# Optimization experiments

Measured on AMD Instinct MI355X. Metric: run time of the kernel, lower is better.

## Reference

```python
import jax, jax.numpy as jnp
import numpy as np

FEATURE_DIM, HIDDEN_DIM, ATTN_DIM = 2048, 1024, 1024
B, L = 128, 196


def setup_inputs() -> dict:
    key = jax.random.key(0)
    ks = jax.random.split(key, 8)
    s_enc = 1.0 / np.sqrt(FEATURE_DIM)
    s_hid = 1.0 / np.sqrt(HIDDEN_DIM)
    s_full = 1.0 / np.sqrt(ATTN_DIM)
    return {
        "encoder_out": jax.random.normal(ks[0], (B, L, FEATURE_DIM), jnp.float32),
        "hidden": jax.random.normal(ks[1], (B, HIDDEN_DIM), jnp.float32),
        "W_enc": jax.random.uniform(ks[2], (FEATURE_DIM, ATTN_DIM), jnp.float32, -s_enc, s_enc),
        "b_enc": jax.random.uniform(ks[3], (ATTN_DIM,), jnp.float32, -s_enc, s_enc),
        "W_hid": jax.random.uniform(ks[4], (HIDDEN_DIM, ATTN_DIM), jnp.float32, -s_hid, s_hid),
        "b_hid": jax.random.uniform(ks[5], (ATTN_DIM,), jnp.float32, -s_hid, s_hid),
        "W_full": jax.random.uniform(ks[6], (ATTN_DIM,), jnp.float32, -s_full, s_full),
        "b_full": jax.random.uniform(ks[7], (1,), jnp.float32, -s_full, s_full),
    }


def reference(encoder_out, hidden, W_enc, b_enc, W_hid, b_hid, W_full, b_full):
    # attn1: (B, L, A)
    attn1 = jnp.einsum("blf,fa->bla", encoder_out, W_enc) + b_enc
    # attn2: (B, 1, A)
    attn2 = (hidden @ W_hid + b_hid)[:, None, :]
    attn = jax.nn.relu(attn1 + attn2)
    # scalar score per location: (B, L)
    scores = jnp.einsum("bla,a->bl", attn, W_full) + b_full[0]
    alpha = jax.nn.softmax(scores, axis=1)
    # weighted sum over L: (B, F)
    context = jnp.einsum("blf,bl->bf", encoder_out, alpha)
    return context, alpha
```

## Files before the change

kernel.cpp:

```cpp
#include <hip/hip_runtime.h>
#include <hip/hip_bf16.h>

typedef unsigned short u16;
typedef short s16x8 __attribute__((ext_vector_type(8)));
typedef unsigned int u32x2 __attribute__((ext_vector_type(2)));
typedef float f32x4 __attribute__((ext_vector_type(4)));

#define F_DIM 2048
#define A_DIM 1024
#define H_DIM 1024
#define BATCH 128
#define LLEN  196
#define MROWS (BATCH * LLEN)
#define MTILES (MROWS / 256)

__device__ __forceinline__ u16 f2b(float x) {
  union { float f; unsigned int u; } c; c.f = x;
  unsigned int r = (c.u + 0x7fffu + ((c.u >> 16) & 1u)) >> 16;
  return (u16)r;
}

__device__ __forceinline__ unsigned int f2b_pk(float a, float b) {
  unsigned int r;
  asm volatile("v_cvt_pk_bf16_f32 %0, %1, %2" : "=v"(r) : "v"(a), "v"(b));
  return r;
}

__device__ __forceinline__ void gload_lds16(const void* g, void* l) {
  __builtin_amdgcn_global_load_lds((const __attribute__((address_space(1))) void*)g,
                                   (__attribute__((address_space(3))) void*)l, 16, 0, 0);
}

__global__ void wenc_cvt_kernel(const float* __restrict__ W, u16* __restrict__ WT) {
  __shared__ float tile[32][33];
  int kb = blockIdx.x * 32, ab = blockIdx.y * 32;
  int t = threadIdx.x;
  int r = t >> 3, c = (t & 7) * 4;
  float4 v = *(const float4*)&W[(size_t)(kb + r) * A_DIM + ab + c];
  tile[r][c] = v.x; tile[r][c + 1] = v.y; tile[r][c + 2] = v.z; tile[r][c + 3] = v.w;
  __syncthreads();
  ushort4 o;
  o.x = f2b(tile[c + 0][r]);
  o.y = f2b(tile[c + 1][r]);
  o.z = f2b(tile[c + 2][r]);
  o.w = f2b(tile[c + 3][r]);
  *(ushort4*)&WT[(size_t)(ab + r) * F_DIM + kb + c] = o;
}

__global__ void attn2_kernel(const float* __restrict__ hidden, const float* __restrict__ W_hid,
                             const float* __restrict__ b_hid, const float* __restrict__ b_enc,
                             float* __restrict__ attn2p) {
  __shared__ float hl[8][128];
  int t = threadIdx.x;
  int a  = blockIdx.x * 256 + t;
  int b0 = blockIdx.y * 8;
  int k0 = blockIdx.z * 128;
  {
    int j = t >> 5, kk = (t & 31) * 4;
    float4 v = *(const float4*)&hidden[(size_t)(b0 + j) * H_DIM + k0 + kk];
    hl[j][kk + 0] = v.x; hl[j][kk + 1] = v.y; hl[j][kk + 2] = v.z; hl[j][kk + 3] = v.w;
  }
  __syncthreads();
  float acc[8] = {0.f, 0.f, 0.f, 0.f, 0.f, 0.f, 0.f, 0.f};
  #pragma unroll 4
  for (int k = 0; k < 128; ++k) {
    float w = W_hid[(size_t)(k0 + k) * A_DIM + a];
    #pragma unroll
    for (int j = 0; j < 8; ++j) acc[j] = fmaf(hl[j][k], w, acc[j]);
  }
  if (blockIdx.z == 0) {
    float bias = b_hid[a] + b_enc[a];
    #pragma unroll
    for (int j = 0; j < 8; ++j) acc[j] += bias;
  }
  #pragma unroll
  for (int j = 0; j < 8; ++j) atomicAdd(&attn2p[(size_t)(b0 + j) * A_DIM + a], acc[j]);
}

__global__ __launch_bounds__(512, 2) void gemm_score(
    const float* __restrict__ enc, const u16* __restrict__ WT,
    const float* __restrict__ attn2p, const float* __restrict__ W_full,
    float* __restrict__ scores) {
  __shared__ __align__(16) u16 As[4 * 8192];
  __shared__ __align__(16) u16 Bs[4 * 8192];

  int i = blockIdx.x;
  int g = i >> 5, r = i & 31;
  int y = r >> 3, gi = r & 7;
  int mt = g * 8 + gi;
  if (mt >= MTILES) return;
  int m0 = mt * 256, n0 = y * 256;
  int t = threadIdx.x;
  int lane = t & 63, wave = t >> 6;
  int wr = wave >> 2, wc = wave & 3;
  int c16 = lane & 15, quad = lane >> 4;

  const float* aP = enc + (size_t)(m0 + (t >> 3)) * F_DIM + (t & 7) * 4;
  const int awoff = (t >> 3) * 32 + ((((t & 7) >> 1) ^ (((t >> 3) >> 1) & 3)) * 8)
                  + ((t & 7) & 1) * 4;
  const u16* bP = WT + (size_t)(n0 + (t >> 2)) * F_DIM + ((t & 3) ^ ((t >> 3) & 3)) * 8;
  const int bw512 = wave * 512;

  const int akey = (c16 >> 1) & 3;
  const int aroff = (wr * 128 + c16) * 32 + (quad ^ akey) * 8;
  const int broff = (wc * 64 + c16) * 32 + (quad ^ akey) * 8;

  f32x4 acc[8][4];
  #pragma unroll
  for (int mi = 0; mi < 8; ++mi)
    #pragma unroll
    for (int ni = 0; ni < 4; ++ni) acc[mi][ni] = (f32x4){0.f, 0.f, 0.f, 0.f};

  float4 R0[4], R1[4];

  #pragma unroll
  for (int ii = 0; ii < 4; ++ii) R0[ii] = *(const float4*)(aP + (size_t)ii * 64 * F_DIM);
  #pragma unroll
  for (int ii = 0; ii < 4; ++ii) R1[ii] = *(const float4*)(aP + (size_t)ii * 64 * F_DIM + 32);
  gload_lds16(bP, &Bs[bw512]);
  gload_lds16(bP + (size_t)128 * F_DIM, &Bs[4096 + bw512]);
  gload_lds16(bP + 32, &Bs[8192 + bw512]);
  gload_lds16(bP + (size_t)128 * F_DIM + 32, &Bs[8192 + 4096 + bw512]);
  #pragma unroll
  for (int ii = 0; ii < 4; ++ii) {
    u32x2 w; w.x = f2b_pk(R0[ii].x, R0[ii].y); w.y = f2b_pk(R0[ii].z, R0[ii].w);
    *(u32x2*)&As[awoff + ii * 2048] = w;
  }
  #pragma unroll
  for (int ii = 0; ii < 4; ++ii) {
    u32x2 w; w.x = f2b_pk(R1[ii].x, R1[ii].y); w.y = f2b_pk(R1[ii].z, R1[ii].w);
    *(u32x2*)&As[8192 + awoff + ii * 2048] = w;
  }
  #pragma unroll
  for (int ii = 0; ii < 4; ++ii) R0[ii] = *(const float4*)(aP + (size_t)ii * 64 * F_DIM + 64);
  #pragma unroll
  for (int ii = 0; ii < 4; ++ii) R1[ii] = *(const float4*)(aP + (size_t)ii * 64 * F_DIM + 96);
  asm volatile("s_waitcnt vmcnt(0) lgkmcnt(0)" ::: "memory");
  __builtin_amdgcn_s_barrier();

#define TILE(J, RX) do {                                                        \
    const int rb_ = (J) * 8192;                                                 \
    const int wb_ = (((J) + 2) & 3) * 8192;                                     \
    int p_ = kt + (J);                                                          \
    int kts_ = min(p_ + 2, 63);                                                 \
    int ktl_ = min(p_ + 4, 63);                                                 \
    _Pragma("unroll")                                                           \
    for (int ii = 0; ii < 4; ++ii) {                                            \
      u32x2 w_; w_.x = f2b_pk(RX[ii].x, RX[ii].y);                              \
      w_.y = f2b_pk(RX[ii].z, RX[ii].w);                                        \
      *(u32x2*)&As[wb_ + awoff + ii * 2048] = w_;                               \
    }                                                                           \
    _Pragma("unroll")                                                           \
    for (int ii = 0; ii < 4; ++ii)                                              \
      RX[ii] = *(const float4*)(aP + (size_t)ii * 64 * F_DIM + ktl_ * 32);      \
    gload_lds16(bP + (size_t)kts_ * 32, &Bs[wb_ + bw512]);                      \
    gload_lds16(bP + (size_t)128 * F_DIM + (size_t)kts_ * 32,                   \
                &Bs[wb_ + 4096 + bw512]);                                       \
    {                                                                           \
      s16x8 af_[8], bf_[4];                                                     \
      _Pragma("unroll")                                                         \
      for (int ni = 0; ni < 4; ++ni)                                            \
        bf_[ni] = *(const s16x8*)&Bs[rb_ + broff + ni * 512];                   \
      _Pragma("unroll")                                                         \
      for (int mi = 0; mi < 8; ++mi)                                            \
        af_[mi] = *(const s16x8*)&As[rb_ + aroff + mi * 512];                   \
      __builtin_amdgcn_s_setprio(1);                                            \
      _Pragma("unroll")                                                         \
      for (int mi = 0; mi < 8; ++mi)                                            \
        _Pragma("unroll")                                                       \
        for (int ni = 0; ni < 4; ++ni)                                          \
          acc[mi][ni] = __builtin_amdgcn_mfma_f32_16x16x32_bf16(                \
              af_[mi], bf_[ni], acc[mi][ni], 0, 0, 0);                          \
      __builtin_amdgcn_s_setprio(0);                                            \
    }                                                                           \
    asm volatile("s_waitcnt vmcnt(6) lgkmcnt(0)" ::: "memory");                 \
    __builtin_amdgcn_s_barrier();                                               \
  } while (0)

  #pragma unroll 1
  for (int kt = 0; kt < 64; kt += 4) {
    TILE(0, R0);
    TILE(1, R1);
    TILE(2, R0);
    TILE(3, R1);
  }
#undef TILE

  int bfirst = m0 / LLEN;
  int bnd1 = (bfirst + 1) * LLEN, bnd2 = (bfirst + 2) * LLEN;
  int b1c = min(bfirst + 1, BATCH - 1), b2c = min(bfirst + 2, BATCH - 1);
  float wf[4], a2v0[4], a2v1[4], a2v2[4];
  #pragma unroll
  for (int ni = 0; ni < 4; ++ni) {
    int col = n0 + wc * 64 + ni * 16 + c16;
    wf[ni]   = W_full[col];
    a2v0[ni] = attn2p[(size_t)bfirst * A_DIM + col];
    a2v1[ni] = attn2p[(size_t)b1c * A_DIM + col];
    a2v2[ni] = attn2p[(size_t)b2c * A_DIM + col];
  }
  #pragma unroll
  for (int mi = 0; mi < 8; ++mi) {
    #pragma unroll
    for (int rr = 0; rr < 4; ++rr) {
      int row_g = m0 + wr * 128 + mi * 16 + quad * 4 + rr;
      float p = 0.f;
      #pragma unroll
      for (int ni = 0; ni < 4; ++ni) {
        float a2 = row_g >= bnd1 ? (row_g >= bnd2 ? a2v2[ni] : a2v1[ni]) : a2v0[ni];
        float v = acc[mi][ni][rr] + a2;
        v = fmaxf(v, 0.f);
        p = fmaf(v, wf[ni], p);
      }
      p += __shfl_xor(p, 1);
      p += __shfl_xor(p, 2);
      p += __shfl_xor(p, 4);
      p += __shfl_xor(p, 8);
      if (c16 == 0) atomicAdd(&scores[row_g], p);
    }
  }
}

__global__ void softmax_kernel(const float* __restrict__ scores, float* __restrict__ alpha) {
  __shared__ float red[8];
  int b = blockIdx.x, t = threadIdx.x;
  float s = (t < LLEN) ? scores[b * LLEN + t] : -3.0e38f;
  float m = s;
  #pragma unroll
  for (int o = 1; o <= 32; o <<= 1) m = fmaxf(m, __shfl_xor(m, o));
  if ((t & 63) == 0) red[t >> 6] = m;
  __syncthreads();
  m = fmaxf(fmaxf(red[0], red[1]), fmaxf(red[2], red[3]));
  float e = (t < LLEN) ? expf(s - m) : 0.f;
  float sum = e;
  #pragma unroll
  for (int o = 1; o <= 32; o <<= 1) sum += __shfl_xor(sum, o);
  __syncthreads();
  if ((t & 63) == 0) red[4 + (t >> 6)] = sum;
  __syncthreads();
  sum = red[4] + red[5] + red[6] + red[7];
  if (t < LLEN) alpha[b * LLEN + t] = e / sum;
}

__global__ void context_kernel(const float* __restrict__ enc, const float* __restrict__ alpha,
                               float* __restrict__ out) {
  __shared__ float al[49];
  int b = blockIdx.y, t = threadIdx.x;
  int l0 = blockIdx.z * 49;
  int f4 = blockIdx.x * 256 + t;
  if (t < 49) al[t] = alpha[b * LLEN + l0 + t];
  __syncthreads();
  const float4* e4 = (const float4*)enc + ((size_t)b * LLEN + l0) * (F_DIM / 4) + f4;
  float4 acc = {0.f, 0.f, 0.f, 0.f};
  #pragma unroll 7
  for (int l = 0; l < 49; ++l) {
    float4 v = e4[(size_t)l * (F_DIM / 4)];
    float a = al[l];
    acc.x = fmaf(v.x, a, acc.x);
    acc.y = fmaf(v.y, a, acc.y);
    acc.z = fmaf(v.z, a, acc.z);
    acc.w = fmaf(v.w, a, acc.w);
  }
  float* o = out + (size_t)b * F_DIM + f4 * 4;
  atomicAdd(o + 0, acc.x);
  atomicAdd(o + 1, acc.y);
  atomicAdd(o + 2, acc.z);
  atomicAdd(o + 3, acc.w);
}

extern "C" void kernel_launch(void* const* d_in, const int* in_sizes, int n_in,
                              void* d_out, int out_size, void* d_ws, size_t ws_size,
                              hipStream_t stream) {
  const float* enc    = (const float*)d_in[0];
  const float* hidden = (const float*)d_in[1];
  const float* W_enc  = (const float*)d_in[2];
  const float* b_enc  = (const float*)d_in[3];
  const float* W_hid  = (const float*)d_in[4];
  const float* b_hid  = (const float*)d_in[5];
  const float* W_full = (const float*)d_in[6];
  float* out = (float*)d_out;
  float* alpha_out = out + (size_t)BATCH * F_DIM;

  const size_t wt_bytes = (size_t)A_DIM * F_DIM * sizeof(u16);
  const size_t a2_bytes = (size_t)BATCH * A_DIM * sizeof(float);
  const size_t sc_bytes = (size_t)MROWS * sizeof(float);
  char* ws = (char*)d_ws;
  u16*   WT     = (u16*)ws;
  float* attn2p = (float*)(ws + wt_bytes);
  float* scores = (float*)(ws + wt_bytes + a2_bytes);

  hipMemsetAsync(attn2p, 0, a2_bytes, stream);
  hipMemsetAsync(scores, 0, sc_bytes, stream);
  hipMemsetAsync(out, 0, (size_t)BATCH * F_DIM * sizeof(float), stream);

  wenc_cvt_kernel<<<dim3(F_DIM / 32, A_DIM / 32), 256, 0, stream>>>(W_enc, WT);
  attn2_kernel<<<dim3(A_DIM / 256, BATCH / 8, H_DIM / 128), 256, 0, stream>>>(hidden, W_hid, b_hid, b_enc, attn2p);
  gemm_score<<<dim3(416), 512, 0, stream>>>(enc, WT, attn2p, W_full, scores);
  softmax_kernel<<<dim3(BATCH), 256, 0, stream>>>(scores, alpha_out);
  context_kernel<<<dim3(2, BATCH, 4), 256, 0, stream>>>(enc, alpha_out, out);
}
```

Measured before the change: 493.0 us.

## Restructure score GEMM to double-buffered K=64 tiles with phased MFMA pipeline

The main GEMM moves from four-stage K=32 LDS buffers to two-stage K=64 buffers with an 8-bit XOR swizzle. Each tile is split into four phases that interleave global loads, bf16 conversion writes and MFMA quadrants, with barriers between phases, to overlap memory traffic with compute. The context kernel now handles the full sequence per block and writes with a plain store, which removes the atomics and the output memset, and two memsets are merged into one. The price is fewer context blocks (256), which lowers parallelism, plus extra barriers in the GEMM.

```diff
diff --git a/kernel.cpp b/kernel.cpp
--- a/kernel.cpp
+++ b/kernel.cpp
@@ -81,8 +81,8 @@
     const float* __restrict__ enc, const u16* __restrict__ WT,
     const float* __restrict__ attn2p, const float* __restrict__ W_full,
     float* __restrict__ scores) {
-  __shared__ __align__(16) u16 As[4 * 8192];
-  __shared__ __align__(16) u16 Bs[4 * 8192];
+  __shared__ __align__(16) u16 As[2 * 16384];
+  __shared__ __align__(16) u16 Bs[2 * 16384];
 
   int i = blockIdx.x;
   int g = i >> 5, r = i & 31;
@@ -95,15 +95,20 @@
   int wr = wave >> 2, wc = wave & 3;
   int c16 = lane & 15, quad = lane >> 4;
 
-  const float* aP = enc + (size_t)(m0 + (t >> 3)) * F_DIM + (t & 7) * 4;
-  const int awoff = (t >> 3) * 32 + ((((t & 7) >> 1) ^ (((t >> 3) >> 1) & 3)) * 8)
-                  + ((t & 7) & 1) * 4;
-  const u16* bP = WT + (size_t)(n0 + (t >> 2)) * F_DIM + ((t & 3) ^ ((t >> 3) & 3)) * 8;
-  const int bw512 = wave * 512;
-
-  const int akey = (c16 >> 1) & 3;
-  const int aroff = (wr * 128 + c16) * 32 + (quad ^ akey) * 8;
-  const int broff = (wc * 64 + c16) * 32 + (quad ^ akey) * 8;
+  const float* aP = enc + (size_t)(m0 + (t >> 2)) * F_DIM + (t & 3) * 4;
+  int awo[4];
+  #pragma unroll
+  for (int s = 0; s < 4; ++s)
+    awo[s] = (t >> 2) * 64 + ((t & 3) & 1) * 4
+           + (((s * 2 + ((t & 3) >> 1)) ^ ((t >> 2) & 7)) * 8);
+  const u16* bgp = WT + (size_t)(n0 + (t >> 3)) * F_DIM + ((t & 7) ^ ((t >> 3) & 7)) * 8;
+
+  const int akey = c16 & 7;
+  int gsw[2];
+  gsw[0] = ((0 * 4 + quad) ^ akey) * 8;
+  gsw[1] = ((1 * 4 + quad) ^ akey) * 8;
+  const int aro = (wr * 128 + c16) * 64;
+  const int bro = (wc * 64 + c16) * 64;
 
   f32x4 acc[8][4];
   #pragma unroll
@@ -111,80 +116,104 @@
     #pragma unroll
     for (int ni = 0; ni < 4; ++ni) acc[mi][ni] = (f32x4){0.f, 0.f, 0.f, 0.f};
 
-  float4 R0[4], R1[4];
-
-  #pragma unroll
-  for (int ii = 0; ii < 4; ++ii) R0[ii] = *(const float4*)(aP + (size_t)ii * 64 * F_DIM);
-  #pragma unroll
-  for (int ii = 0; ii < 4; ++ii) R1[ii] = *(const float4*)(aP + (size_t)ii * 64 * F_DIM + 32);
-  gload_lds16(bP, &Bs[bw512]);
-  gload_lds16(bP + (size_t)128 * F_DIM, &Bs[4096 + bw512]);
-  gload_lds16(bP + 32, &Bs[8192 + bw512]);
-  gload_lds16(bP + (size_t)128 * F_DIM + 32, &Bs[8192 + 4096 + bw512]);
-  #pragma unroll
-  for (int ii = 0; ii < 4; ++ii) {
-    u32x2 w; w.x = f2b_pk(R0[ii].x, R0[ii].y); w.y = f2b_pk(R0[ii].z, R0[ii].w);
-    *(u32x2*)&As[awoff + ii * 2048] = w;
-  }
-  #pragma unroll
-  for (int ii = 0; ii < 4; ++ii) {
-    u32x2 w; w.x = f2b_pk(R1[ii].x, R1[ii].y); w.y = f2b_pk(R1[ii].z, R1[ii].w);
-    *(u32x2*)&As[8192 + awoff + ii * 2048] = w;
-  }
-  #pragma unroll
-  for (int ii = 0; ii < 4; ++ii) R0[ii] = *(const float4*)(aP + (size_t)ii * 64 * F_DIM + 64);
-  #pragma unroll
-  for (int ii = 0; ii < 4; ++ii) R1[ii] = *(const float4*)(aP + (size_t)ii * 64 * F_DIM + 96);
+  s16x8 af[4][2], bf[2][2];
+  float4 RAlo[4], RAhi[4];
+
+#define ALD(RX, half, kt_) do {                                                 \
+    const float* p_ = aP + (size_t)(half) * 128 * F_DIM + (kt_) * 64;           \
+    RX[0] = *(const float4*)(p_);                                               \
+    RX[1] = *(const float4*)(p_ + 16);                                          \
+    RX[2] = *(const float4*)(p_ + 32);                                          \
+    RX[3] = *(const float4*)(p_ + 48);                                          \
+  } while (0)
+
+#define AWR(RX, cb, half) do {                                                  \
+    _Pragma("unroll")                                                           \
+    for (int s_ = 0; s_ < 4; ++s_) {                                            \
+      u32x2 w_; w_.x = f2b_pk(RX[s_].x, RX[s_].y);                              \
+      w_.y = f2b_pk(RX[s_].z, RX[s_].w);                                        \
+      *(u32x2*)&As[(cb) * 16384 + (half) * 8192 + awo[s_]] = w_;                \
+    }                                                                           \
+  } while (0)
+
+#define BGL(cb, kt_) do {                                                       \
+    _Pragma("unroll")                                                           \
+    for (int s_ = 0; s_ < 4; ++s_)                                              \
+      gload_lds16(bgp + (size_t)s_ * 64 * F_DIM + (size_t)(kt_) * 64,           \
+                  Bs + (cb) * 16384 + s_ * 4096 + wave * 512);                  \
+  } while (0)
+
+#define DSRA(cb, mh)                                                            \
+    _Pragma("unroll")                                                           \
+    for (int i_ = 0; i_ < 4; ++i_)                                              \
+      _Pragma("unroll")                                                         \
+      for (int h_ = 0; h_ < 2; ++h_)                                            \
+        af[i_][h_] = *(const s16x8*)&As[(cb) * 16384 + aro                      \
+                                        + ((mh) * 4 + i_) * 1024 + gsw[h_]];
+
+#define DSRB(cb, nh)                                                            \
+    _Pragma("unroll")                                                           \
+    for (int j_ = 0; j_ < 2; ++j_)                                              \
+      _Pragma("unroll")                                                         \
+      for (int h_ = 0; h_ < 2; ++h_)                                            \
+        bf[j_][h_] = *(const s16x8*)&Bs[(cb) * 16384 + bro                      \
+                                        + ((nh) * 2 + j_) * 1024 + gsw[h_]];
+
+#define GATE8 asm volatile("s_waitcnt vmcnt(8)" ::: "memory")
+#define NOGATE ((void)0)
+
+#define PHASE(cb, mh, nh, GATE, ...) do {                                       \
+    if ((nh) == 0) { DSRA(cb, mh); }                                            \
+    DSRB(cb, nh);                                                               \
+    __VA_ARGS__                                                                 \
+    GATE;                                                                       \
+    __builtin_amdgcn_s_barrier();                                               \
+    asm volatile("s_waitcnt lgkmcnt(0)" ::: "memory");                          \
+    __builtin_amdgcn_s_setprio(1);                                              \
+    _Pragma("unroll")                                                           \
+    for (int i_ = 0; i_ < 4; ++i_)                                              \
+      _Pragma("unroll")                                                         \
+      for (int j_ = 0; j_ < 2; ++j_)                                            \
+        _Pragma("unroll")                                                       \
+        for (int h_ = 0; h_ < 2; ++h_)                                          \
+          acc[(mh) * 4 + i_][(nh) * 2 + j_] =                                   \
+              __builtin_amdgcn_mfma_f32_16x16x32_bf16(                          \
+                  af[i_][h_], bf[j_][h_],                                       \
+                  acc[(mh) * 4 + i_][(nh) * 2 + j_], 0, 0, 0);                  \
+    __builtin_amdgcn_s_setprio(0);                                              \
+    __builtin_amdgcn_s_barrier();                                               \
+  } while (0)
+
+  BGL(0, 0);
+  ALD(RAlo, 0, 0);
+  ALD(RAhi, 1, 0);
+  AWR(RAlo, 0, 0);
+  AWR(RAhi, 0, 1);
+  ALD(RAlo, 0, 1);
+  AWR(RAlo, 1, 0);
+  ALD(RAhi, 1, 1);
   asm volatile("s_waitcnt vmcnt(0) lgkmcnt(0)" ::: "memory");
   __builtin_amdgcn_s_barrier();
 
-#define TILE(J, RX) do {                                                        \
-    const int rb_ = (J) * 8192;                                                 \
-    const int wb_ = (((J) + 2) & 3) * 8192;                                     \
-    int p_ = kt + (J);                                                          \
-    int kts_ = min(p_ + 2, 63);                                                 \
-    int ktl_ = min(p_ + 4, 63);                                                 \
-    _Pragma("unroll")                                                           \
-    for (int ii = 0; ii < 4; ++ii) {                                            \
-      u32x2 w_; w_.x = f2b_pk(RX[ii].x, RX[ii].y);                              \
-      w_.y = f2b_pk(RX[ii].z, RX[ii].w);                                        \
-      *(u32x2*)&As[wb_ + awoff + ii * 2048] = w_;                               \
-    }                                                                           \
-    _Pragma("unroll")                                                           \
-    for (int ii = 0; ii < 4; ++ii)                                              \
-      RX[ii] = *(const float4*)(aP + (size_t)ii * 64 * F_DIM + ktl_ * 32);      \
-    gload_lds16(bP + (size_t)kts_ * 32, &Bs[wb_ + bw512]);                      \
-    gload_lds16(bP + (size_t)128 * F_DIM + (size_t)kts_ * 32,                   \
-                &Bs[wb_ + 4096 + bw512]);                                       \
-    {                                                                           \
-      s16x8 af_[8], bf_[4];                                                     \
-      _Pragma("unroll")                                                         \
-      for (int ni = 0; ni < 4; ++ni)                                            \
-        bf_[ni] = *(const s16x8*)&Bs[rb_ + broff + ni * 512];                   \
-      _Pragma("unroll")                                                         \
-      for (int mi = 0; mi < 8; ++mi)                                            \
-        af_[mi] = *(const s16x8*)&As[rb_ + aroff + mi * 512];                   \
-      __builtin_amdgcn_s_setprio(1);                                            \
-      _Pragma("unroll")                                                         \
-      for (int mi = 0; mi < 8; ++mi)                                            \
-        _Pragma("unroll")                                                       \
-        for (int ni = 0; ni < 4; ++ni)                                          \
-          acc[mi][ni] = __builtin_amdgcn_mfma_f32_16x16x32_bf16(                \
-              af_[mi], bf_[ni], acc[mi][ni], 0, 0, 0);                          \
-      __builtin_amdgcn_s_setprio(0);                                            \
-    }                                                                           \
-    asm volatile("s_waitcnt vmcnt(6) lgkmcnt(0)" ::: "memory");                 \
-    __builtin_amdgcn_s_barrier();                                               \
-  } while (0)
-
   #pragma unroll 1
-  for (int kt = 0; kt < 64; kt += 4) {
-    TILE(0, R0);
-    TILE(1, R1);
-    TILE(2, R0);
-    TILE(3, R1);
-  }
-#undef TILE
+  for (int it = 0; it < 16; ++it) {
+    int tt = 2 * it;
+    int t2 = min(tt + 2, 31), t3 = min(tt + 3, 31);
+    PHASE(0, 0, 0, NOGATE, AWR(RAhi, 1, 1); BGL(1, tt + 1););
+    PHASE(0, 0, 1, NOGATE, ALD(RAlo, 0, t2););
+    PHASE(0, 1, 0, NOGATE, ALD(RAhi, 1, t2););
+    PHASE(0, 1, 1, GATE8,  AWR(RAlo, 0, 0););
+    PHASE(1, 0, 0, NOGATE, AWR(RAhi, 0, 1); BGL(0, t2););
+    PHASE(1, 0, 1, NOGATE, ALD(RAlo, 0, t3););
+    PHASE(1, 1, 0, NOGATE, ALD(RAhi, 1, t3););
+    PHASE(1, 1, 1, GATE8,  AWR(RAlo, 1, 0););
+  }
+#undef PHASE
+#undef DSRA
+#undef DSRB
+#undef BGL
+#undef AWR
+#undef ALD
 
   int bfirst = m0 / LLEN;
   int bnd1 = (bfirst + 1) * LLEN, bnd2 = (bfirst + 2) * LLEN;
@@ -241,18 +270,18 @@
   if (t < LLEN) alpha[b * LLEN + t] = e / sum;
 }
 
-__global__ void context_kernel(const float* __restrict__ enc, const float* __restrict__ alpha,
-                               float* __restrict__ out) {
-  __shared__ float al[49];
+__global__ __launch_bounds__(256) void context_kernel(
+    const float* __restrict__ enc, const float* __restrict__ alpha,
+    float* __restrict__ out) {
+  __shared__ float al[LLEN];
   int b = blockIdx.y, t = threadIdx.x;
-  int l0 = blockIdx.z * 49;
+  if (t < LLEN) al[t] = alpha[b * LLEN + t];
+  __syncthreads();
   int f4 = blockIdx.x * 256 + t;
-  if (t < 49) al[t] = alpha[b * LLEN + l0 + t];
-  __syncthreads();
-  const float4* e4 = (const float4*)enc + ((size_t)b * LLEN + l0) * (F_DIM / 4) + f4;
+  const float4* e4 = (const float4*)enc + (size_t)b * LLEN * (F_DIM / 4) + f4;
   float4 acc = {0.f, 0.f, 0.f, 0.f};
-  #pragma unroll 7
-  for (int l = 0; l < 49; ++l) {
+  #pragma unroll 4
+  for (int l = 0; l < LLEN; ++l) {
     float4 v = e4[(size_t)l * (F_DIM / 4)];
     float a = al[l];
     acc.x = fmaf(v.x, a, acc.x);
@@ -260,11 +289,7 @@
     acc.z = fmaf(v.z, a, acc.z);
     acc.w = fmaf(v.w, a, acc.w);
   }
-  float* o = out + (size_t)b * F_DIM + f4 * 4;
-  atomicAdd(o + 0, acc.x);
-  atomicAdd(o + 1, acc.y);
-  atomicAdd(o + 2, acc.z);
-  atomicAdd(o + 3, acc.w);
+  *(float4*)(out + (size_t)b * F_DIM + f4 * 4) = acc;
 }
 
 extern "C" void kernel_launch(void* const* d_in, const int* in_sizes, int n_in,
@@ -288,13 +313,11 @@
   float* attn2p = (float*)(ws + wt_bytes);
   float* scores = (float*)(ws + wt_bytes + a2_bytes);
 
-  hipMemsetAsync(attn2p, 0, a2_bytes, stream);
-  hipMemsetAsync(scores, 0, sc_bytes, stream);
-  hipMemsetAsync(out, 0, (size_t)BATCH * F_DIM * sizeof(float), stream);
+  hipMemsetAsync(attn2p, 0, a2_bytes + sc_bytes, stream);
 
   wenc_cvt_kernel<<<dim3(F_DIM / 32, A_DIM / 32), 256, 0, stream>>>(W_enc, WT);
   attn2_kernel<<<dim3(A_DIM / 256, BATCH / 8, H_DIM / 128), 256, 0, stream>>>(hidden, W_hid, b_hid, b_enc, attn2p);
   gemm_score<<<dim3(416), 512, 0, stream>>>(enc, WT, attn2p, W_full, scores);
   softmax_kernel<<<dim3(BATCH), 256, 0, stream>>>(scores, alpha_out);
-  context_kernel<<<dim3(2, BATCH, 4), 256, 0, stream>>>(enc, alpha_out, out);
-}
+  context_kernel<<<dim3(2, BATCH), 256, 0, stream>>>(enc, alpha_out, out);
+}
```

Measured after the change: 480.2 us. 2.6% less time.
